# Performance work log

Hardware: AMD Instinct MI355X
Metric: run time of the kernel (lower is better)

The kernel has to match this reference:

```python
import jax, jax.numpy as jnp
import numpy as np
import itertools

EPS = 1e-6
# Blade ordering for Cl(3,0): (), e1,e2,e3, e12,e13,e23, e123 -> grade of each blade
GRADE = np.array([0, 1, 1, 1, 2, 2, 2, 3])
_SL = [(0, 1), (1, 4), (4, 7), (7, 8)]  # blade slices per grade subspace


def build_cayley():
    """Geometric-product Cayley table for Cl(3,0) (Euclidean metric)."""
    blades = [()] + [c for r in range(1, 4) for c in itertools.combinations(range(3), r)]
    masks = [sum(1 << i for i in b) for b in blades]
    idx = {m: i for i, m in enumerate(masks)}
    C = np.zeros((8, 8, 8), np.float32)
    for i, a in enumerate(masks):
        for j, b in enumerate(masks):
            s, aa = 0, a >> 1
            while aa:
                s += bin(aa & b).count('1')
                aa >>= 1
            C[i, j, idx[a ^ b]] = -1.0 if (s & 1) else 1.0
    return C


def _qs(x):
    """Quadratic form per grade subspace: [..., 8] -> [..., 4] (Euclidean metric)."""
    x2 = x * x
    return jnp.concatenate([x2[..., a:b].sum(-1, keepdims=True) for a, b in _SL], axis=-1)


def _mvlinear(x, w, b=None):
    """Per-subspace multivector linear. x: [B, m, 8], w: [n, m, 4], b: [n] (scalar blade)."""
    out = jnp.einsum('bmi,nmi->bni', x, w[:, :, GRADE])
    if b is not None:
        out = out.at[..., 0].add(b)
    return out


def setup_inputs() -> dict:
    key = jax.random.key(0)
    ks = jax.random.split(key, 12)
    B, Fin, Fout = 131072, 16, 32
    return dict(
        x=jax.random.normal(ks[0], (B, Fin, 8), jnp.float32),
        w1=jax.random.normal(ks[1], (Fout, Fin, 4), jnp.float32) * float(1.0 / np.sqrt(Fin)),
        b1=jax.random.normal(ks[2], (Fout,), jnp.float32) * 0.1,
        a_relu=jax.random.uniform(ks[3], (Fout, 4), jnp.float32) + 0.5,
        b_relu=jax.random.normal(ks[4], (Fout, 4), jnp.float32) * 0.1,
        wl=jax.random.normal(ks[5], (Fout, Fout, 4), jnp.float32) * float(1.0 / np.sqrt(Fout)),
        bl=jax.random.normal(ks[6], (Fout,), jnp.float32) * 0.1,
        wr=jax.random.normal(ks[7], (Fout, Fout, 4), jnp.float32) * float(1.0 / np.sqrt(Fout)),
        a_norm=jax.random.normal(ks[8], (Fout, 4), jnp.float32) * 0.1,
        gp_w=jax.random.normal(ks[9], (Fout, 4, 4, 4), jnp.float32) * 0.5,
        a_ln=jax.random.uniform(ks[10], (Fout,), jnp.float32) + 0.5,
        cayley=jnp.asarray(build_cayley()),
    )


def reference(x, w1, b1, a_relu, b_relu, wl, bl, wr, a_norm, gp_w, a_ln, cayley):
    # --- MVLinear ---
    h = _mvlinear(x, w1, b1)  # [B, C, 8]
    # --- MVReLU: gate each channel by relu(a * invariants + b), invariants broadcast per grade ---
    inv = jnp.concatenate([h[..., :1], _qs(h)[..., 1:]], axis=-1)  # [B, C, 4]
    h = jax.nn.relu(a_relu * inv + b_relu)[..., GRADE] * h
    # --- SteerableGeometricProductLayer ---
    xr = _mvlinear(h, wr)  # linear_right (no bias)
    n = jnp.sqrt(jnp.abs(_qs(xr)))  # grade-wise norms
    n = jax.nn.sigmoid(a_norm) * (n - 1.0) + 1.0  # learned interpolation toward unit norm
    xr = xr / (n[..., GRADE] + EPS)
    # per-channel steerable geometric product weight: cayley * grade-block weight
    W = cayley[None] * gp_w[:, GRADE][:, :, GRADE][:, :, :, GRADE]  # [C, 8, 8, 8]
    h = (_mvlinear(h, wl, bl) + jnp.einsum('bci,cijk,bck->bcj', h, W, xr)) * float(1.0 / np.sqrt(2.0))
    # --- MVLayerNorm: divide by channel-mean multivector norm ---
    nrm = jnp.sqrt(_qs(h).sum(-1, keepdims=True)).mean(axis=1, keepdims=True) + EPS  # [B, 1, 1]
    return a_ln[:, None] * h / nrm
```

## Files before the change

kernel.cpp:

```cpp
#include <hip/hip_runtime.h>
#include <math.h>

#define EPSV 1e-6f

namespace {

constexpr int FIN   = 16;
constexpr int FOUT  = 32;
constexpr int EPT   = 2;
constexpr int ELEMS = 8 * EPT;
constexpr int BLK   = 256;
constexpr int GRID  = 1024;

constexpr int GJ[8][8] = {
  {0,1,2,3,4,5,6,7},
  {1,0,4,5,2,3,7,6},
  {2,4,0,6,1,7,3,5},
  {3,5,6,0,7,1,2,4},
  {4,2,1,7,0,6,5,3},
  {5,3,7,1,6,0,4,2},
  {6,7,3,2,5,4,0,1},
  {7,6,5,4,3,2,1,0},
};
constexpr float SREF[8][8] = {
  { 1, 1, 1, 1, 1, 1, 1, 1},
  { 1, 1, 1, 1, 1, 1, 1, 1},
  { 1,-1, 1, 1,-1,-1, 1,-1},
  { 1,-1,-1, 1, 1,-1,-1, 1},
  {-1, 1,-1,-1, 1, 1,-1, 1},
  {-1, 1, 1,-1,-1, 1, 1,-1},
  {-1,-1, 1,-1, 1,-1, 1, 1},
  {-1,-1, 1,-1, 1,-1, 1, 1},
};
constexpr int GSLOT[8][8] = {
  {0,1,1,1,2,2,2,3},
  {5,4,7,7,6,6,9,8},
  {5,7,4,7,6,9,6,8},
  {5,7,7,4,9,6,6,8},
  {13,11,11,15,10,14,14,12},
  {13,11,15,11,14,10,14,12},
  {13,15,11,11,14,14,10,12},
  {19,18,18,18,17,17,17,16},
};
constexpr int SLOT_OFF[20] = {0,5,10,15,17,20,22,25,27,30,34,37,39,40,42,45,51,54,57,60};

}

__global__ __launch_bounds__(BLK, 4)
void cge_block_kernel(const float* __restrict__ x,
                      const float* __restrict__ w1,
                      const float* __restrict__ b1,
                      const float* __restrict__ a_relu,
                      const float* __restrict__ b_relu,
                      const float* __restrict__ wl,
                      const float* __restrict__ bl,
                      const float* __restrict__ wr,
                      const float* __restrict__ a_norm,
                      const float* __restrict__ gp_w,
                      const float* __restrict__ a_ln,
                      float* __restrict__ out,
                      int B)
{
  __shared__ float4 w1s[FIN * FOUT];
  __shared__ float4 wrs[FOUT * FOUT];
  __shared__ float4 hs[2][ELEMS * FOUT];

  const int tid  = threadIdx.x;
  const int c    = tid & 31;
  const int slot = tid >> 5;

  for (int idx = tid; idx < FIN * FOUT; idx += BLK) {
    int cc = idx >> 4, m = idx & 15;
    w1s[m * FOUT + cc] = ((const float4*)w1)[idx];
  }
  for (int idx = tid; idx < FOUT * FOUT; idx += BLK) {
    int cc = idx >> 5, m = idx & 31;
    wrs[m * FOUT + cc] = ((const float4*)wr)[idx];
  }

  float gw[20];
#pragma unroll
  for (int s = 0; s < 20; ++s) gw[s] = gp_w[c * 64 + SLOT_OFF[s]];
  const float  b1c  = b1[c];
  const float  blc  = bl[c];
  const float  alnc = a_ln[c];
  const float4 ar   = ((const float4*)a_relu)[c];
  const float4 br   = ((const float4*)b_relu)[c];
  const float4 an   = ((const float4*)a_norm)[c];
  const float  sg0  = 1.f / (1.f + expf(-an.x));
  const float  sg1  = 1.f / (1.f + expf(-an.y));
  const float  sg2  = 1.f / (1.f + expf(-an.z));
  const float  sg3  = 1.f / (1.f + expf(-an.w));
  const float4* wlc = ((const float4*)wl) + c * FOUT;

  const int ngroups = B / ELEMS;
  const float4* xg = (const float4*)x;

  __syncthreads();

  for (int g = blockIdx.x; g < ngroups; g += gridDim.x) {
    const int eb = g * ELEMS;

    float h0[EPT][8];
#pragma unroll
    for (int e = 0; e < EPT; ++e) {
      h0[e][0] = b1c;
#pragma unroll
      for (int i = 1; i < 8; ++i) h0[e][i] = 0.f;
    }
#pragma unroll 4
    for (int m = 0; m < FIN; ++m) {
      const float4 w = w1s[m * FOUT + c];
#pragma unroll
      for (int e = 0; e < EPT; ++e) {
        const int le = slot * EPT + e;
        const size_t base = (size_t)(eb + le) * (FIN * 2) + m * 2;
        const float4 xlo = xg[base];
        const float4 xhi = xg[base + 1];
        h0[e][0] += xlo.x * w.x;
        h0[e][1] += xlo.y * w.y;
        h0[e][2] += xlo.z * w.y;
        h0[e][3] += xlo.w * w.y;
        h0[e][4] += xhi.x * w.z;
        h0[e][5] += xhi.y * w.z;
        h0[e][6] += xhi.z * w.z;
        h0[e][7] += xhi.w * w.w;
      }
    }

    __syncthreads();

#pragma unroll
    for (int e = 0; e < EPT; ++e) {
      const int le = slot * EPT + e;
      const float q1 = h0[e][1]*h0[e][1] + h0[e][2]*h0[e][2] + h0[e][3]*h0[e][3];
      const float q2 = h0[e][4]*h0[e][4] + h0[e][5]*h0[e][5] + h0[e][6]*h0[e][6];
      const float q3 = h0[e][7]*h0[e][7];
      const float g0 = fmaxf(ar.x * h0[e][0] + br.x, 0.f);
      const float g1 = fmaxf(ar.y * q1 + br.y, 0.f);
      const float g2 = fmaxf(ar.z * q2 + br.z, 0.f);
      const float g3 = fmaxf(ar.w * q3 + br.w, 0.f);
      h0[e][0] *= g0;
      h0[e][1] *= g1; h0[e][2] *= g1; h0[e][3] *= g1;
      h0[e][4] *= g2; h0[e][5] *= g2; h0[e][6] *= g2;
      h0[e][7] *= g3;
      hs[0][le * FOUT + c] = make_float4(h0[e][0], h0[e][1], h0[e][2], h0[e][3]);
      hs[1][le * FOUT + c] = make_float4(h0[e][4], h0[e][5], h0[e][6], h0[e][7]);
    }
    __syncthreads();

    float xr[EPT][8];
    float h2[EPT][8];
#pragma unroll
    for (int e = 0; e < EPT; ++e) {
      h2[e][0] = blc;
#pragma unroll
      for (int i = 1; i < 8; ++i) h2[e][i] = 0.f;
#pragma unroll
      for (int i = 0; i < 8; ++i) xr[e][i] = 0.f;
    }
#pragma unroll 4
    for (int m = 0; m < FOUT; ++m) {
      const float4 wrv = wrs[m * FOUT + c];
      const float4 wlv = wlc[m];
#pragma unroll
      for (int e = 0; e < EPT; ++e) {
        const int le = slot * EPT + e;
        const float4 hlo = hs[0][le * FOUT + m];
        const float4 hhi = hs[1][le * FOUT + m];
        xr[e][0] += hlo.x * wrv.x;
        xr[e][1] += hlo.y * wrv.y;
        xr[e][2] += hlo.z * wrv.y;
        xr[e][3] += hlo.w * wrv.y;
        xr[e][4] += hhi.x * wrv.z;
        xr[e][5] += hhi.y * wrv.z;
        xr[e][6] += hhi.z * wrv.z;
        xr[e][7] += hhi.w * wrv.w;
        h2[e][0] += hlo.x * wlv.x;
        h2[e][1] += hlo.y * wlv.y;
        h2[e][2] += hlo.z * wlv.y;
        h2[e][3] += hlo.w * wlv.y;
        h2[e][4] += hhi.x * wlv.z;
        h2[e][5] += hhi.y * wlv.z;
        h2[e][6] += hhi.z * wlv.z;
        h2[e][7] += hhi.w * wlv.w;
      }
    }

#pragma unroll
    for (int e = 0; e < EPT; ++e) {
      const float q0 = xr[e][0]*xr[e][0];
      const float q1 = xr[e][1]*xr[e][1] + xr[e][2]*xr[e][2] + xr[e][3]*xr[e][3];
      const float q2 = xr[e][4]*xr[e][4] + xr[e][5]*xr[e][5] + xr[e][6]*xr[e][6];
      const float q3 = xr[e][7]*xr[e][7];
      const float r0 = 1.f / (sg0 * (sqrtf(q0) - 1.f) + 1.f + EPSV);
      const float r1 = 1.f / (sg1 * (sqrtf(q1) - 1.f) + 1.f + EPSV);
      const float r2 = 1.f / (sg2 * (sqrtf(q2) - 1.f) + 1.f + EPSV);
      const float r3 = 1.f / (sg3 * (sqrtf(q3) - 1.f) + 1.f + EPSV);
      xr[e][0] *= r0;
      xr[e][1] *= r1; xr[e][2] *= r1; xr[e][3] *= r1;
      xr[e][4] *= r2; xr[e][5] *= r2; xr[e][6] *= r2;
      xr[e][7] *= r3;
    }

#pragma unroll
    for (int i = 0; i < 8; ++i) {
#pragma unroll
      for (int k = 0; k < 8; ++k) {
        const float w = SREF[i][k] * gw[GSLOT[i][k]];
#pragma unroll
        for (int e = 0; e < EPT; ++e) {
          h2[e][GJ[i][k]] += (w * h0[e][i]) * xr[e][k];
        }
      }
    }

#pragma unroll
    for (int e = 0; e < EPT; ++e) {
      const int le = slot * EPT + e;
      float s = 0.f;
#pragma unroll
      for (int i = 0; i < 8; ++i) {
        h2[e][i] *= 0.70710678118654752f;
        s += h2[e][i] * h2[e][i];
      }
      float n = sqrtf(s);
      n += __shfl_xor(n, 1);
      n += __shfl_xor(n, 2);
      n += __shfl_xor(n, 4);
      n += __shfl_xor(n, 8);
      n += __shfl_xor(n, 16);
      const float scale = alnc / (n * (1.f / FOUT) + EPSV);
      float4* o4 = (float4*)out + (size_t)(eb + le) * (FOUT * 2) + c * 2;
      o4[0] = make_float4(h2[e][0] * scale, h2[e][1] * scale,
                          h2[e][2] * scale, h2[e][3] * scale);
      o4[1] = make_float4(h2[e][4] * scale, h2[e][5] * scale,
                          h2[e][6] * scale, h2[e][7] * scale);
    }
  }
}

extern "C" void kernel_launch(void* const* d_in, const int* in_sizes, int n_in,
                              void* d_out, int out_size, void* d_ws, size_t ws_size,
                              hipStream_t stream) {
  const float* x      = (const float*)d_in[0];
  const float* w1     = (const float*)d_in[1];
  const float* b1     = (const float*)d_in[2];
  const float* a_relu = (const float*)d_in[3];
  const float* b_relu = (const float*)d_in[4];
  const float* wl     = (const float*)d_in[5];
  const float* bl     = (const float*)d_in[6];
  const float* wr     = (const float*)d_in[7];
  const float* a_norm = (const float*)d_in[8];
  const float* gp_w   = (const float*)d_in[9];
  const float* a_ln   = (const float*)d_in[10];

  const int B = in_sizes[0] / (FIN * 8);
  const int ngroups = B / ELEMS;
  const int grid = ngroups < GRID ? ngroups : GRID;

  cge_block_kernel<<<grid, BLK, 0, stream>>>(
      x, w1, b1, a_relu, b_relu, wl, bl, wr, a_norm, gp_w, a_ln,
      (float*)d_out, B);
}
```

Baseline: 442.9 us.

## Remap threads to two channels each, bf16-pack LDS staging, prefetch x

Each thread now handles two channels of one element instead of one channel of two elements. The input x is prefetched one group ahead into a double-buffered LDS tile. The intermediate h tile in LDS and the staged x are stored as packed bf16 to halve LDS traffic and footprint. The grid and occupancy hint change from 1024 blocks at 4 waves to 768 blocks at 3. Packing x and h to bf16 lowers precision and may break tolerance, and wl is still read from global memory.

```diff
diff --git a/kernel.cpp b/kernel.cpp
--- a/kernel.cpp
+++ b/kernel.cpp
@@ -7,10 +7,9 @@
 
 constexpr int FIN   = 16;
 constexpr int FOUT  = 32;
-constexpr int EPT   = 2;
-constexpr int ELEMS = 8 * EPT;
 constexpr int BLK   = 256;
-constexpr int GRID  = 1024;
+constexpr int ELEMS = 16;
+constexpr int GRID  = 768;
 
 constexpr int GJ[8][8] = {
   {0,1,2,3,4,5,6,7},
@@ -44,9 +43,23 @@
 };
 constexpr int SLOT_OFF[20] = {0,5,10,15,17,20,22,25,27,30,34,37,39,40,42,45,51,54,57,60};
 
-}
-
-__global__ __launch_bounds__(BLK, 4)
+__device__ __forceinline__ unsigned bfp(float a) {
+  union { float f; unsigned u; } v; v.f = a;
+  return (v.u + 0x7fffu + ((v.u >> 16) & 1u)) >> 16;
+}
+__device__ __forceinline__ unsigned pk2(float a, float b) {
+  return bfp(a) | (bfp(b) << 16);
+}
+__device__ __forceinline__ float blo(unsigned d) {
+  union { unsigned u; float f; } v; v.u = d << 16; return v.f;
+}
+__device__ __forceinline__ float bhi(unsigned d) {
+  union { unsigned u; float f; } v; v.u = d & 0xffff0000u; return v.f;
+}
+
+}
+
+__global__ __launch_bounds__(BLK, 3)
 void cge_block_kernel(const float* __restrict__ x,
                       const float* __restrict__ w1,
                       const float* __restrict__ b1,
@@ -63,11 +76,13 @@
 {
   __shared__ float4 w1s[FIN * FOUT];
   __shared__ float4 wrs[FOUT * FOUT];
-  __shared__ float4 hs[2][ELEMS * FOUT];
+  __shared__ uint4  xsb[2][ELEMS * FIN];
+  __shared__ uint4  hsb[ELEMS * FOUT];
 
   const int tid  = threadIdx.x;
-  const int c    = tid & 31;
-  const int slot = tid >> 5;
+  const int cidx = tid & 15;
+  const int le   = tid >> 4;
+  const int c0   = cidx, c1 = cidx + 16;
 
   for (int idx = tid; idx < FIN * FOUT; idx += BLK) {
     int cc = idx >> 4, m = idx & 15;
@@ -78,165 +93,169 @@
     wrs[m * FOUT + cc] = ((const float4*)wr)[idx];
   }
 
-  float gw[20];
-#pragma unroll
-  for (int s = 0; s < 20; ++s) gw[s] = gp_w[c * 64 + SLOT_OFF[s]];
-  const float  b1c  = b1[c];
-  const float  blc  = bl[c];
-  const float  alnc = a_ln[c];
-  const float4 ar   = ((const float4*)a_relu)[c];
-  const float4 br   = ((const float4*)b_relu)[c];
-  const float4 an   = ((const float4*)a_norm)[c];
-  const float  sg0  = 1.f / (1.f + expf(-an.x));
-  const float  sg1  = 1.f / (1.f + expf(-an.y));
-  const float  sg2  = 1.f / (1.f + expf(-an.z));
-  const float  sg3  = 1.f / (1.f + expf(-an.w));
-  const float4* wlc = ((const float4*)wl) + c * FOUT;
+  float gw[2][20];
+  float arr[2][4], brr[2][4], sgg[2][4];
+  float b1c[2], blc[2], alnc[2];
+  const int cs[2] = {c0, c1};
+#pragma unroll
+  for (int t = 0; t < 2; ++t) {
+    const int c = cs[t];
+#pragma unroll
+    for (int s = 0; s < 20; ++s) gw[t][s] = gp_w[c * 64 + SLOT_OFF[s]];
+    const float4 ar = ((const float4*)a_relu)[c];
+    const float4 br = ((const float4*)b_relu)[c];
+    const float4 an = ((const float4*)a_norm)[c];
+    arr[t][0]=ar.x; arr[t][1]=ar.y; arr[t][2]=ar.z; arr[t][3]=ar.w;
+    brr[t][0]=br.x; brr[t][1]=br.y; brr[t][2]=br.z; brr[t][3]=br.w;
+    sgg[t][0]=1.f/(1.f+expf(-an.x)); sgg[t][1]=1.f/(1.f+expf(-an.y));
+    sgg[t][2]=1.f/(1.f+expf(-an.z)); sgg[t][3]=1.f/(1.f+expf(-an.w));
+    b1c[t]=b1[c]; blc[t]=bl[c]; alnc[t]=a_ln[c];
+  }
+  const float4* wlg = (const float4*)wl;
+  const float4* xg4 = (const float4*)x;
 
   const int ngroups = B / ELEMS;
-  const float4* xg = (const float4*)x;
-
+  const int stride  = gridDim.x;
+  const int g0      = blockIdx.x;
+
+  float4 px0, px1;
+  auto issue_x = [&](int g) {
+    const size_t bi = ((size_t)(g * ELEMS + le) * FIN + cidx) * 2;
+    px0 = xg4[bi]; px1 = xg4[bi + 1];
+  };
+
+  issue_x(g0 < ngroups ? g0 : 0);
+  xsb[0][le * FIN + cidx] = make_uint4(pk2(px0.x, px0.y), pk2(px0.z, px0.w),
+                                       pk2(px1.x, px1.y), pk2(px1.z, px1.w));
+  { int gn = g0 + stride; if (gn >= ngroups) gn = 0; issue_x(gn); }
   __syncthreads();
 
-  for (int g = blockIdx.x; g < ngroups; g += gridDim.x) {
+  int p = 0;
+  for (int g = g0; g < ngroups; g += stride, p ^= 1) {
     const int eb = g * ELEMS;
 
-    float h0[EPT][8];
-#pragma unroll
-    for (int e = 0; e < EPT; ++e) {
-      h0[e][0] = b1c;
-#pragma unroll
-      for (int i = 1; i < 8; ++i) h0[e][i] = 0.f;
+    float h0[2][8];
+#pragma unroll
+    for (int t = 0; t < 2; ++t) {
+      h0[t][0] = b1c[t];
+#pragma unroll
+      for (int i = 1; i < 8; ++i) h0[t][i] = 0.f;
     }
 #pragma unroll 4
     for (int m = 0; m < FIN; ++m) {
-      const float4 w = w1s[m * FOUT + c];
-#pragma unroll
-      for (int e = 0; e < EPT; ++e) {
-        const int le = slot * EPT + e;
-        const size_t base = (size_t)(eb + le) * (FIN * 2) + m * 2;
-        const float4 xlo = xg[base];
-        const float4 xhi = xg[base + 1];
-        h0[e][0] += xlo.x * w.x;
-        h0[e][1] += xlo.y * w.y;
-        h0[e][2] += xlo.z * w.y;
-        h0[e][3] += xlo.w * w.y;
-        h0[e][4] += xhi.x * w.z;
-        h0[e][5] += xhi.y * w.z;
-        h0[e][6] += xhi.z * w.z;
-        h0[e][7] += xhi.w * w.w;
-      }
-    }
-
+      const uint4 xb = xsb[p][le * FIN + m];
+      const float x0 = blo(xb.x), x1 = bhi(xb.x), x2 = blo(xb.y), x3 = bhi(xb.y);
+      const float x4 = blo(xb.z), x5 = bhi(xb.z), x6 = blo(xb.w), x7 = bhi(xb.w);
+      const float4 wa = w1s[m * FOUT + c0];
+      const float4 wb = w1s[m * FOUT + c1];
+      h0[0][0] += x0*wa.x; h0[0][1] += x1*wa.y; h0[0][2] += x2*wa.y; h0[0][3] += x3*wa.y;
+      h0[0][4] += x4*wa.z; h0[0][5] += x5*wa.z; h0[0][6] += x6*wa.z; h0[0][7] += x7*wa.w;
+      h0[1][0] += x0*wb.x; h0[1][1] += x1*wb.y; h0[1][2] += x2*wb.y; h0[1][3] += x3*wb.y;
+      h0[1][4] += x4*wb.z; h0[1][5] += x5*wb.z; h0[1][6] += x6*wb.z; h0[1][7] += x7*wb.w;
+    }
+
+#pragma unroll
+    for (int t = 0; t < 2; ++t) {
+      const float q1 = h0[t][1]*h0[t][1] + h0[t][2]*h0[t][2] + h0[t][3]*h0[t][3];
+      const float q2 = h0[t][4]*h0[t][4] + h0[t][5]*h0[t][5] + h0[t][6]*h0[t][6];
+      const float q3 = h0[t][7]*h0[t][7];
+      const float g0v = fmaxf(arr[t][0] * h0[t][0] + brr[t][0], 0.f);
+      const float g1v = fmaxf(arr[t][1] * q1 + brr[t][1], 0.f);
+      const float g2v = fmaxf(arr[t][2] * q2 + brr[t][2], 0.f);
+      const float g3v = fmaxf(arr[t][3] * q3 + brr[t][3], 0.f);
+      h0[t][0] *= g0v;
+      h0[t][1] *= g1v; h0[t][2] *= g1v; h0[t][3] *= g1v;
+      h0[t][4] *= g2v; h0[t][5] *= g2v; h0[t][6] *= g2v;
+      h0[t][7] *= g3v;
+    }
+
+    hsb[le * FOUT + c0] = make_uint4(pk2(h0[0][0], h0[0][1]), pk2(h0[0][2], h0[0][3]),
+                                     pk2(h0[0][4], h0[0][5]), pk2(h0[0][6], h0[0][7]));
+    hsb[le * FOUT + c1] = make_uint4(pk2(h0[1][0], h0[1][1]), pk2(h0[1][2], h0[1][3]),
+                                     pk2(h0[1][4], h0[1][5]), pk2(h0[1][6], h0[1][7]));
+    xsb[p ^ 1][le * FIN + cidx] = make_uint4(pk2(px0.x, px0.y), pk2(px0.z, px0.w),
+                                             pk2(px1.x, px1.y), pk2(px1.z, px1.w));
+    { int gn = g + 2 * stride; if (gn >= ngroups) gn = g0; issue_x(gn); }
     __syncthreads();
 
-#pragma unroll
-    for (int e = 0; e < EPT; ++e) {
-      const int le = slot * EPT + e;
-      const float q1 = h0[e][1]*h0[e][1] + h0[e][2]*h0[e][2] + h0[e][3]*h0[e][3];
-      const float q2 = h0[e][4]*h0[e][4] + h0[e][5]*h0[e][5] + h0[e][6]*h0[e][6];
-      const float q3 = h0[e][7]*h0[e][7];
-      const float g0 = fmaxf(ar.x * h0[e][0] + br.x, 0.f);
-      const float g1 = fmaxf(ar.y * q1 + br.y, 0.f);
-      const float g2 = fmaxf(ar.z * q2 + br.z, 0.f);
-      const float g3 = fmaxf(ar.w * q3 + br.w, 0.f);
-      h0[e][0] *= g0;
-      h0[e][1] *= g1; h0[e][2] *= g1; h0[e][3] *= g1;
-      h0[e][4] *= g2; h0[e][5] *= g2; h0[e][6] *= g2;
-      h0[e][7] *= g3;
-      hs[0][le * FOUT + c] = make_float4(h0[e][0], h0[e][1], h0[e][2], h0[e][3]);
-      hs[1][le * FOUT + c] = make_float4(h0[e][4], h0[e][5], h0[e][6], h0[e][7]);
-    }
-    __syncthreads();
-
-    float xr[EPT][8];
-    float h2[EPT][8];
-#pragma unroll
-    for (int e = 0; e < EPT; ++e) {
-      h2[e][0] = blc;
-#pragma unroll
-      for (int i = 1; i < 8; ++i) h2[e][i] = 0.f;
-#pragma unroll
-      for (int i = 0; i < 8; ++i) xr[e][i] = 0.f;
+    float xr[2][8], h2[2][8];
+#pragma unroll
+    for (int t = 0; t < 2; ++t) {
+      h2[t][0] = blc[t];
+#pragma unroll
+      for (int i = 1; i < 8; ++i) h2[t][i] = 0.f;
+#pragma unroll
+      for (int i = 0; i < 8; ++i) xr[t][i] = 0.f;
     }
 #pragma unroll 4
     for (int m = 0; m < FOUT; ++m) {
-      const float4 wrv = wrs[m * FOUT + c];
-      const float4 wlv = wlc[m];
-#pragma unroll
-      for (int e = 0; e < EPT; ++e) {
-        const int le = slot * EPT + e;
-        const float4 hlo = hs[0][le * FOUT + m];
-        const float4 hhi = hs[1][le * FOUT + m];
-        xr[e][0] += hlo.x * wrv.x;
-        xr[e][1] += hlo.y * wrv.y;
-        xr[e][2] += hlo.z * wrv.y;
-        xr[e][3] += hlo.w * wrv.y;
-        xr[e][4] += hhi.x * wrv.z;
-        xr[e][5] += hhi.y * wrv.z;
-        xr[e][6] += hhi.z * wrv.z;
-        xr[e][7] += hhi.w * wrv.w;
-        h2[e][0] += hlo.x * wlv.x;
-        h2[e][1] += hlo.y * wlv.y;
-        h2[e][2] += hlo.z * wlv.y;
-        h2[e][3] += hlo.w * wlv.y;
-        h2[e][4] += hhi.x * wlv.z;
-        h2[e][5] += hhi.y * wlv.z;
-        h2[e][6] += hhi.z * wlv.z;
-        h2[e][7] += hhi.w * wlv.w;
+      const uint4 hb = hsb[le * FOUT + m];
+      const float v0 = blo(hb.x), v1 = bhi(hb.x), v2 = blo(hb.y), v3 = bhi(hb.y);
+      const float v4 = blo(hb.z), v5 = bhi(hb.z), v6 = blo(hb.w), v7 = bhi(hb.w);
+      const float4 wra = wrs[m * FOUT + c0];
+      const float4 wrb = wrs[m * FOUT + c1];
+      const float4 wla = wlg[c0 * FOUT + m];
+      const float4 wlb = wlg[c1 * FOUT + m];
+      xr[0][0] += v0*wra.x; xr[0][1] += v1*wra.y; xr[0][2] += v2*wra.y; xr[0][3] += v3*wra.y;
+      xr[0][4] += v4*wra.z; xr[0][5] += v5*wra.z; xr[0][6] += v6*wra.z; xr[0][7] += v7*wra.w;
+      xr[1][0] += v0*wrb.x; xr[1][1] += v1*wrb.y; xr[1][2] += v2*wrb.y; xr[1][3] += v3*wrb.y;
+      xr[1][4] += v4*wrb.z; xr[1][5] += v5*wrb.z; xr[1][6] += v6*wrb.z; xr[1][7] += v7*wrb.w;
+      h2[0][0] += v0*wla.x; h2[0][1] += v1*wla.y; h2[0][2] += v2*wla.y; h2[0][3] += v3*wla.y;
+      h2[0][4] += v4*wla.z; h2[0][5] += v5*wla.z; h2[0][6] += v6*wla.z; h2[0][7] += v7*wla.w;
+      h2[1][0] += v0*wlb.x; h2[1][1] += v1*wlb.y; h2[1][2] += v2*wlb.y; h2[1][3] += v3*wlb.y;
+      h2[1][4] += v4*wlb.z; h2[1][5] += v5*wlb.z; h2[1][6] += v6*wlb.z; h2[1][7] += v7*wlb.w;
+    }
+
+#pragma unroll
+    for (int t = 0; t < 2; ++t) {
+      const float q0 = xr[t][0]*xr[t][0];
+      const float q1 = xr[t][1]*xr[t][1] + xr[t][2]*xr[t][2] + xr[t][3]*xr[t][3];
+      const float q2 = xr[t][4]*xr[t][4] + xr[t][5]*xr[t][5] + xr[t][6]*xr[t][6];
+      const float q3 = xr[t][7]*xr[t][7];
+      const float r0 = 1.f / (sgg[t][0] * (sqrtf(q0) - 1.f) + 1.f + EPSV);
+      const float r1 = 1.f / (sgg[t][1] * (sqrtf(q1) - 1.f) + 1.f + EPSV);
+      const float r2 = 1.f / (sgg[t][2] * (sqrtf(q2) - 1.f) + 1.f + EPSV);
+      const float r3 = 1.f / (sgg[t][3] * (sqrtf(q3) - 1.f) + 1.f + EPSV);
+      xr[t][0] *= r0;
+      xr[t][1] *= r1; xr[t][2] *= r1; xr[t][3] *= r1;
+      xr[t][4] *= r2; xr[t][5] *= r2; xr[t][6] *= r2;
+      xr[t][7] *= r3;
+    }
+
+#pragma unroll
+    for (int i = 0; i < 8; ++i) {
+#pragma unroll
+      for (int k = 0; k < 8; ++k) {
+        const int j = GJ[i][k], s = GSLOT[i][k];
+        h2[0][j] += (SREF[i][k] * gw[0][s] * h0[0][i]) * xr[0][k];
+        h2[1][j] += (SREF[i][k] * gw[1][s] * h0[1][i]) * xr[1][k];
       }
     }
 
-#pragma unroll
-    for (int e = 0; e < EPT; ++e) {
-      const float q0 = xr[e][0]*xr[e][0];
-      const float q1 = xr[e][1]*xr[e][1] + xr[e][2]*xr[e][2] + xr[e][3]*xr[e][3];
-      const float q2 = xr[e][4]*xr[e][4] + xr[e][5]*xr[e][5] + xr[e][6]*xr[e][6];
-      const float q3 = xr[e][7]*xr[e][7];
-      const float r0 = 1.f / (sg0 * (sqrtf(q0) - 1.f) + 1.f + EPSV);
-      const float r1 = 1.f / (sg1 * (sqrtf(q1) - 1.f) + 1.f + EPSV);
-      const float r2 = 1.f / (sg2 * (sqrtf(q2) - 1.f) + 1.f + EPSV);
-      const float r3 = 1.f / (sg3 * (sqrtf(q3) - 1.f) + 1.f + EPSV);
-      xr[e][0] *= r0;
-      xr[e][1] *= r1; xr[e][2] *= r1; xr[e][3] *= r1;
-      xr[e][4] *= r2; xr[e][5] *= r2; xr[e][6] *= r2;
-      xr[e][7] *= r3;
-    }
-
-#pragma unroll
-    for (int i = 0; i < 8; ++i) {
-#pragma unroll
-      for (int k = 0; k < 8; ++k) {
-        const float w = SREF[i][k] * gw[GSLOT[i][k]];
-#pragma unroll
-        for (int e = 0; e < EPT; ++e) {
-          h2[e][GJ[i][k]] += (w * h0[e][i]) * xr[e][k];
-        }
+    float s = 0.f;
+#pragma unroll
+    for (int t = 0; t < 2; ++t) {
+      float q = 0.f;
+#pragma unroll
+      for (int i = 0; i < 8; ++i) {
+        h2[t][i] *= 0.70710678118654752f;
+        q += h2[t][i] * h2[t][i];
       }
-    }
-
-#pragma unroll
-    for (int e = 0; e < EPT; ++e) {
-      const int le = slot * EPT + e;
-      float s = 0.f;
-#pragma unroll
-      for (int i = 0; i < 8; ++i) {
-        h2[e][i] *= 0.70710678118654752f;
-        s += h2[e][i] * h2[e][i];
-      }
-      float n = sqrtf(s);
-      n += __shfl_xor(n, 1);
-      n += __shfl_xor(n, 2);
-      n += __shfl_xor(n, 4);
-      n += __shfl_xor(n, 8);
-      n += __shfl_xor(n, 16);
-      const float scale = alnc / (n * (1.f / FOUT) + EPSV);
-      float4* o4 = (float4*)out + (size_t)(eb + le) * (FOUT * 2) + c * 2;
-      o4[0] = make_float4(h2[e][0] * scale, h2[e][1] * scale,
-                          h2[e][2] * scale, h2[e][3] * scale);
-      o4[1] = make_float4(h2[e][4] * scale, h2[e][5] * scale,
-                          h2[e][6] * scale, h2[e][7] * scale);
-    }
+      s += sqrtf(q);
+    }
+    s += __shfl_xor(s, 1);
+    s += __shfl_xor(s, 2);
+    s += __shfl_xor(s, 4);
+    s += __shfl_xor(s, 8);
+    const float nrm = s * (1.f / FOUT) + EPSV;
+    float4* o4 = (float4*)out + (size_t)(eb + le) * (FOUT * 2);
+#pragma unroll
+    for (int t = 0; t < 2; ++t) {
+      const float sc = alnc[t] / nrm;
+      o4[cs[t] * 2]     = make_float4(h2[t][0]*sc, h2[t][1]*sc, h2[t][2]*sc, h2[t][3]*sc);
+      o4[cs[t] * 2 + 1] = make_float4(h2[t][4]*sc, h2[t][5]*sc, h2[t][6]*sc, h2[t][7]*sc);
+    }
+    __syncthreads();
   }
 }
 
```

Measured after the change: 576.8 us. 1.3x slower.
